# Kernel optimization log

Hardware: AMD Instinct MI355X
Metric: run time of the kernel (lower is better)

Reference implementation:

```python
import jax, jax.numpy as jnp
import numpy as np

T, B, V, E = 256, 128, 256, 512
NN = (1024, 1024)  # num_nodes per LSTM layer


def setup_inputs() -> dict:
    key = jax.random.key(0)
    ks = jax.random.split(key, 8)
    inputs = jax.random.normal(ks[0], (T, B, V), jnp.float32)
    emb = jax.random.normal(ks[1], (V, E), jnp.float32) * np.float32(np.sqrt(1.0 / V))
    w0 = jax.random.normal(ks[2], (E + NN[0], 4 * NN[0]), jnp.float32) * np.float32(np.sqrt(1.0 / (E + NN[0])))
    b0 = jnp.zeros((4 * NN[0],), jnp.float32)
    w1 = jax.random.normal(ks[3], (NN[0] + NN[1], 4 * NN[1]), jnp.float32) * np.float32(np.sqrt(1.0 / (NN[0] + NN[1])))
    b1 = jnp.zeros((4 * NN[1],), jnp.float32)
    out_w = jax.random.normal(ks[4], (NN[1], V), jnp.float32) * np.float32(np.sqrt(1.0 / NN[1]))
    out_b = jnp.zeros((V,), jnp.float32)
    return {"inputs": inputs, "embedding_matrix": emb,
            "lstm_w0": w0, "lstm_b0": b0, "lstm_w1": w1, "lstm_b1": b1,
            "out_w": out_w, "out_b": out_b}


def reference(inputs, embedding_matrix, lstm_w0, lstm_b0, lstm_w1, lstm_b1, out_w, out_b):
    Tn, Bn, _ = inputs.shape
    # _embed: (stacked one-hot) @ embedding_matrix -> [T, B, E]
    embs = jnp.einsum('tbv,ve->tbe', inputs, embedding_matrix)
    ws = (lstm_w0, lstm_w1)
    bs = (lstm_b0, lstm_b1)
    init_states = tuple((jnp.zeros((Bn, n), embs.dtype), jnp.zeros((Bn, n), embs.dtype)) for n in NN)

    def step(states, emb):
        out = emb
        new_states = []
        for i in range(len(NN)):
            h, c = states[i]
            n = NN[i]
            # concat([dropout(inp), h]) @ W + b ; dropout_keep_prob = 1.0 -> identity
            lin = jnp.concatenate([out, h], axis=1) @ ws[i] + bs[i]
            f = jax.nn.sigmoid(lin[:, :n])
            ig = jax.nn.sigmoid(lin[:, n:2 * n])
            o = jax.nn.sigmoid(lin[:, 2 * n:3 * n])
            g = jnp.tanh(lin[:, 3 * n:])
            c = f * c + ig * g
            h = o * jnp.tanh(c)
            out = h
            new_states.append((h, c))
        return tuple(new_states), out

    _, rnn_outputs = jax.lax.scan(step, init_states, embs)  # [T, B, NN[-1]]
    # output module: concat over time (axis 0) then single dense layer
    hs = rnn_outputs.reshape(Tn * Bn, NN[-1])
    logits = hs @ out_w + out_b  # [T*B, V]
    return logits
```

## Files before the change

### kernel.cpp

```cpp
#include <hip/hip_runtime.h>
#include <hip/hip_bf16.h>
#include <cstdint>
#include <cstddef>

#define T_STEPS 256
#define BATCH   128
#define VOCAB   256
#define EDIM    512
#define NH      1024
#define GDIM    4096
#define NST0    40
#define NST1    64

typedef __attribute__((ext_vector_type(8))) short short8;
typedef __attribute__((ext_vector_type(4))) float floatx4;

__device__ __forceinline__ float sigmoidf_(float x) { return 1.0f / (1.0f + __expf(-x)); }
__device__ __forceinline__ float tanhf_(float x)    { return 1.0f - 2.0f / (__expf(2.0f * x) + 1.0f); }

typedef __attribute__((address_space(1))) const unsigned int guint;
typedef __attribute__((address_space(3))) unsigned int luint;
__device__ __forceinline__ void load_lds16(const void* g, void* l) {
    __builtin_amdgcn_global_load_lds((guint*)g, (luint*)l, 16, 0, 0);
}

#define BM 128
#define BN 128
#define BK 16
__global__ __launch_bounds__(256) void sgemm_f32(
    const float* __restrict__ A, const float* __restrict__ B,
    float* __restrict__ C, int M, int N, int K)
{
    __shared__ float As[BK][BM + 4];
    __shared__ float Bs[BK][BN + 4];
    const int tid = threadIdx.x;
    const int tr = tid >> 4, tc = tid & 15;
    const int bm = blockIdx.y, bn = blockIdx.x;
    const float* Ab = A + (size_t)bm * BM * K;
    float acc[8][8];
    #pragma unroll
    for (int i = 0; i < 8; ++i)
        #pragma unroll
        for (int j = 0; j < 8; ++j) acc[i][j] = 0.f;
    for (int k0 = 0; k0 < K; k0 += BK) {
        #pragma unroll
        for (int l = 0; l < 2; ++l) {
            int idx = tid + l * 256;
            int row = idx >> 2, c4 = idx & 3;
            float4 v = *(const float4*)(Ab + (size_t)row * K + k0 + c4 * 4);
            As[c4 * 4 + 0][row] = v.x; As[c4 * 4 + 1][row] = v.y;
            As[c4 * 4 + 2][row] = v.z; As[c4 * 4 + 3][row] = v.w;
        }
        #pragma unroll
        for (int l = 0; l < 2; ++l) {
            int idx = tid + l * 256;
            int row = idx >> 5, c4 = idx & 31;
            *(float4*)&Bs[row][c4 * 4] = *(const float4*)(B + (size_t)(k0 + row) * N + bn * BN + c4 * 4);
        }
        __syncthreads();
        #pragma unroll
        for (int kk = 0; kk < BK; ++kk) {
            float4 a0 = *(const float4*)&As[kk][tr * 8];
            float4 a1 = *(const float4*)&As[kk][tr * 8 + 4];
            float4 b0 = *(const float4*)&Bs[kk][tc * 8];
            float4 b1 = *(const float4*)&Bs[kk][tc * 8 + 4];
            float av[8] = {a0.x, a0.y, a0.z, a0.w, a1.x, a1.y, a1.z, a1.w};
            float bv[8] = {b0.x, b0.y, b0.z, b0.w, b1.x, b1.y, b1.z, b1.w};
            #pragma unroll
            for (int i = 0; i < 8; ++i)
                #pragma unroll
                for (int j = 0; j < 8; ++j) acc[i][j] += av[i] * bv[j];
        }
        __syncthreads();
    }
    #pragma unroll
    for (int i = 0; i < 8; ++i) {
        size_t row = (size_t)bm * BM + tr * 8 + i;
        #pragma unroll
        for (int j = 0; j < 8; j += 4) {
            int col = bn * BN + tc * 8 + j;
            *(float4*)(C + row * N + col) =
                make_float4(acc[i][j], acc[i][j+1], acc[i][j+2], acc[i][j+3]);
        }
    }
}

__global__ __launch_bounds__(256) void transpose_to_bf16(
    const float* __restrict__ src, __hip_bfloat16* __restrict__ dst, int R, int C)
{
    __shared__ float t[32][33];
    int x = blockIdx.x * 32 + threadIdx.x;
    #pragma unroll
    for (int i = 0; i < 4; ++i) {
        int y = blockIdx.y * 32 + threadIdx.y + i * 8;
        t[threadIdx.y + i * 8][threadIdx.x] = src[(size_t)y * C + x];
    }
    __syncthreads();
    int x2 = blockIdx.y * 32 + threadIdx.x;
    #pragma unroll
    for (int i = 0; i < 4; ++i) {
        int y2 = blockIdx.x * 32 + threadIdx.y + i * 8;
        dst[(size_t)y2 * R + x2] = __float2bfloat16(t[threadIdx.x][threadIdx.y + i * 8]);
    }
}

__global__ __launch_bounds__(256) void pack_w2(
    const float* __restrict__ src, __hip_bfloat16* __restrict__ dst,
    int koff, int NSTEPS)
{
    __shared__ float t[64][33];
    const int tid = threadIdx.x;
    const int xt = blockIdx.x;
    const int kt = blockIdx.y;
    {
        int yl = tid >> 3;
        int x0 = (tid & 7) * 8;
        const float* p = src + (size_t)(kt * 32 + yl) * GDIM + xt * 64 + x0;
        float4 v0 = *(const float4*)p;
        float4 v1 = *(const float4*)(p + 4);
        t[x0 + 0][yl] = v0.x; t[x0 + 1][yl] = v0.y; t[x0 + 2][yl] = v0.z; t[x0 + 3][yl] = v0.w;
        t[x0 + 4][yl] = v1.x; t[x0 + 5][yl] = v1.y; t[x0 + 6][yl] = v1.z; t[x0 + 7][yl] = v1.w;
    }
    __syncthreads();
    {
        int ll = tid >> 2;
        int quad = tid & 3;
        int lincol = xt * 64 + ll;
        int g = lincol >> 10, n = lincol & 1023;
        int j = n >> 3, c = n & 7;
        int tt = g >> 1;
        int l16 = (g & 1) * 8 + c;
        int s = (koff >> 5) + kt;
        __hip_bfloat16 o[8];
        #pragma unroll
        for (int jj = 0; jj < 8; ++jj)
            o[jj] = __float2bfloat16(t[ll][quad * 8 + jj]);
        size_t off = ((((size_t)j * NSTEPS + s) * 2 + tt) * 64 + (size_t)quad * 16 + l16) * 8;
        *(uint4*)(dst + off) = *(const uint4*)o;
    }
}

__global__ __launch_bounds__(256) void convert_to_bf16(
    const float* __restrict__ src, __hip_bfloat16* __restrict__ dst, size_t n4)
{
    size_t i = (size_t)blockIdx.x * 256 + threadIdx.x;
    if (i < n4) {
        float4 v = *(const float4*)(src + i * 4);
        __hip_bfloat16 o[4] = {__float2bfloat16(v.x), __float2bfloat16(v.y),
                               __float2bfloat16(v.z), __float2bfloat16(v.w)};
        *(uint2*)(dst + i * 4) = *(uint2*)o;
    }
}

#define GKP 40
__global__ __launch_bounds__(256) void gemm_bt(
    const __hip_bfloat16* __restrict__ A, const __hip_bfloat16* __restrict__ Bt,
    const float* __restrict__ bias, float* __restrict__ C, int M, int N, int K)
{
    __shared__ __hip_bfloat16 As[128 * GKP];
    __shared__ __hip_bfloat16 Bs[128 * GKP];
    const int tid = threadIdx.x;
    const int wave = tid >> 6, lane = tid & 63;
    const int quad = lane >> 4, l16 = lane & 15;
    const int wm = (wave >> 1) * 64, wn = (wave & 1) * 64;
    const size_t Arow0 = (size_t)blockIdx.y * 128;
    const size_t Brow0 = (size_t)blockIdx.x * 128;
    floatx4 acc[4][4];
    #pragma unroll
    for (int i = 0; i < 4; ++i)
        #pragma unroll
        for (int j = 0; j < 4; ++j) acc[i][j] = (floatx4)0.f;

    for (int k0 = 0; k0 < K; k0 += 32) {
        #pragma unroll
        for (int l = 0; l < 2; ++l) {
            int idx = tid + l * 256;
            int row = idx >> 2, seg = idx & 3;
            *(uint4*)(As + row * GKP + seg * 8) =
                *(const uint4*)(A + (Arow0 + row) * K + k0 + seg * 8);
            *(uint4*)(Bs + row * GKP + seg * 8) =
                *(const uint4*)(Bt + (Brow0 + row) * K + k0 + seg * 8);
        }
        __syncthreads();
        short8 af[4], bf[4];
        #pragma unroll
        for (int i = 0; i < 4; ++i)
            af[i] = *(const short8*)(As + (wm + i * 16 + l16) * GKP + quad * 8);
        #pragma unroll
        for (int j = 0; j < 4; ++j)
            bf[j] = *(const short8*)(Bs + (wn + j * 16 + l16) * GKP + quad * 8);
        #pragma unroll
        for (int i = 0; i < 4; ++i)
            #pragma unroll
            for (int j = 0; j < 4; ++j)
                acc[i][j] = __builtin_amdgcn_mfma_f32_16x16x32_bf16(af[i], bf[j], acc[i][j], 0, 0, 0);
        __syncthreads();
    }
    #pragma unroll
    for (int i = 0; i < 4; ++i)
        #pragma unroll
        for (int j = 0; j < 4; ++j) {
            int col = (int)Brow0 + wn + j * 16 + l16;
            float bv = bias ? bias[col] : 0.f;
            #pragma unroll
            for (int r = 0; r < 4; ++r) {
                size_t row = Arow0 + wm + i * 16 + quad * 4 + r;
                C[row * N + col] = acc[i][j][r] + bv;
            }
        }
}

struct AfBuf { short8 a[3][8]; };

template<int NCF, int NCS>
__device__ __forceinline__ void chunks_pro(
    AfBuf& B, const __hip_bfloat16* __restrict__ pF,
    const __hip_bfloat16* __restrict__ pS)
{
    constexpr int NC = NCF + NCS;
    constexpr int D = (NC < 3) ? NC : 3;
    #pragma unroll
    for (int c = 0; c < D; ++c) {
        const __hip_bfloat16* pa = (c < NCF) ? (pF + (size_t)c * 256)
                                             : (pS + (size_t)(c - NCF) * 256);
        #pragma unroll
        for (int ss = 0; ss < 8; ++ss)
            B.a[c][ss] = *(const short8*)(pa + ss * 32);
    }
}

template<int NCF, int NCS, int WF, int WS>
__device__ __forceinline__ void chunks_main(
    AfBuf& B, const __hip_bfloat16* __restrict__ pF,
    const __hip_bfloat16* __restrict__ pS,
    const __hip_bfloat16* Wlds, int lane,
    floatx4& acc0, floatx4& acc1)
{
    constexpr int NC = NCF + NCS;
    #pragma unroll
    for (int c = 0; c < NC; ++c) {
        const int wc = (c < NCF) ? (WF + c) : (WS + (c - NCF));
        #pragma unroll
        for (int ss = 0; ss < 8; ++ss) {
            const int s = wc * 8 + ss;
            short8 bf0 = *(const short8*)&Wlds[s * 1024 + lane * 8];
            short8 bf1 = *(const short8*)&Wlds[s * 1024 + 512 + lane * 8];
            acc0 = __builtin_amdgcn_mfma_f32_16x16x32_bf16(B.a[c % 3][ss], bf0, acc0, 0, 0, 0);
            acc1 = __builtin_amdgcn_mfma_f32_16x16x32_bf16(B.a[c % 3][ss], bf1, acc1, 0, 0, 0);
        }
        if (c + 3 < NC) {
            const int cn = c + 3;
            const __hip_bfloat16* pa = (cn < NCF) ? (pF + (size_t)cn * 256)
                                                  : (pS + (size_t)(cn - NCF) * 256);
            #pragma unroll
            for (int ss = 0; ss < 8; ++ss)
                B.a[cn % 3][ss] = *(const short8*)(pa + ss * 32);
        }
    }
}

__global__ __launch_bounds__(512) void lstm_diag(
    const __hip_bfloat16* __restrict__ inbf,
    const __hip_bfloat16* __restrict__ Wpack0,
    const __hip_bfloat16* __restrict__ Wpack1,
    const float* __restrict__ b0, const float* __restrict__ b1,
    __hip_bfloat16* __restrict__ h0_cur,
    const __hip_bfloat16* __restrict__ h0_prev,
    float* __restrict__ c0, float* __restrict__ c1,
    __hip_bfloat16* __restrict__ H1all,
    int d)
{
    const int bid = blockIdx.x;
    const int layer = (bid >> 3) & 1;
    const int j = ((bid >> 4) << 3) | (bid & 7);
    if (layer == 0 && d >= T_STEPS) return;
    if (layer == 1 && d == 0) return;

    __shared__ __attribute__((aligned(16))) __hip_bfloat16 Wlds[65536];

    const int tid = threadIdx.x;
    const int wave = tid >> 6, lane = tid & 63;
    const int quad = lane >> 4, l16 = lane & 15;

    const __hip_bfloat16 *A0, *A1;
    int A0stride;
    const float* bb; float* cst; __hip_bfloat16* hout;
    bool first;
    if (layer == 0) {
        first = (d == 0);
        bb = b0; cst = c0;
        A0 = inbf + (size_t)d * (BATCH * VOCAB); A0stride = VOCAB;
        A1 = h0_prev;
        hout = h0_cur;
        const __hip_bfloat16* Wp = Wpack0 + (size_t)j * (NST0 * 1024);
        #pragma unroll
        for (int it = 0; it < 10; ++it)
            load_lds16(Wp + it * 4096 + tid * 8, Wlds + it * 4096 + tid * 8);
    } else {
        first = (d == 1);
        bb = b1; cst = c1;
        A0 = h0_prev; A0stride = NH;
        A1 = (d >= 2) ? (H1all + (size_t)(d - 2) * (BATCH * NH)) : h0_prev;
        hout = H1all + (size_t)(d - 1) * (BATCH * NH);
        const __hip_bfloat16* Wp = Wpack1 + (size_t)j * (NST1 * 1024);
        #pragma unroll
        for (int it = 0; it < 16; ++it)
            load_lds16(Wp + it * 4096 + tid * 8, Wlds + it * 4096 + tid * 8);
    }

    const int row = wave * 16 + l16;
    const __hip_bfloat16* pA0 = A0 + (size_t)row * A0stride + quad * 8;
    const __hip_bfloat16* pA1 = A1 + (size_t)row * NH + quad * 8;

    const int cc = j * 8 + (l16 & 7);
    float bv0 = bb[((l16 < 8) ? 0 : 1) * NH + cc];
    float bv1 = bb[((l16 < 8) ? 2 : 3) * NH + cc];
    float cold[4];
    {
        const int bbase = 16 * wave + quad * 4;
        #pragma unroll
        for (int r = 0; r < 4; ++r)
            cold[r] = first ? 0.f : cst[(size_t)(bbase + r) * NH + cc];
    }
    floatx4 acc0 = {bv0, bv0, bv0, bv0};
    floatx4 acc1 = {bv1, bv1, bv1, bv1};

    AfBuf B;
    __syncthreads();
    if (layer == 0) {
        if (first) { chunks_pro<1, 0>(B, pA0, pA0); chunks_main<1, 0, 0, 0>(B, pA0, pA0, Wlds, lane, acc0, acc1); }
        else       { chunks_pro<1, 4>(B, pA0, pA1); chunks_main<1, 4, 0, 1>(B, pA0, pA1, Wlds, lane, acc0, acc1); }
    } else {
        if (first) { chunks_pro<4, 0>(B, pA0, pA0); chunks_main<4, 0, 0, 0>(B, pA0, pA0, Wlds, lane, acc0, acc1); }
        else       { chunks_pro<4, 4>(B, pA1, pA0); chunks_main<4, 4, 4, 0>(B, pA1, pA0, Wlds, lane, acc0, acc1); }
    }

    #pragma unroll
    for (int r = 0; r < 4; ++r) {
        float a0 = acc0[r], a1 = acc1[r];
        float p0 = __shfl_xor(a0, 8, 64);
        float p1 = __shfl_xor(a1, 8, 64);
        if (l16 < 8) {
            int b = 16 * wave + quad * 4 + r;
            float f  = sigmoidf_(a0);
            float ig = sigmoidf_(p0);
            float oo = sigmoidf_(a1);
            float gg = tanhf_(p1);
            size_t idx = (size_t)b * NH + cc;
            float cn = f * cold[r] + ig * gg;
            float hn = oo * tanhf_(cn);
            cst[idx] = cn;
            hout[idx] = __float2bfloat16(hn);
        }
    }
}

__device__ __forceinline__ void spin_all_ge(const uint32_t* ep, uint32_t target,
                                            int lane, int wave) {
    asm volatile("" ::: "memory");
    if (wave == 0) {
        for (;;) {
            uint32_t a = __hip_atomic_load(&ep[lane], __ATOMIC_RELAXED, __HIP_MEMORY_SCOPE_AGENT);
            uint32_t b = __hip_atomic_load(&ep[lane + 64], __ATOMIC_RELAXED, __HIP_MEMORY_SCOPE_AGENT);
            if (__all(a >= target && b >= target)) break;
            __builtin_amdgcn_s_sleep(1);
        }
    }
    __builtin_amdgcn_s_barrier();
    asm volatile("" ::: "memory");
}

__device__ __forceinline__ void arrive_ep(uint32_t* slot, uint32_t val) {
    __syncthreads();
    asm volatile("" ::: "memory");
    if (threadIdx.x == 0)
        __hip_atomic_store(slot, val, __ATOMIC_RELAXED, __HIP_MEMORY_SCOPE_AGENT);
}

__global__ void zero_bar(uint32_t* p) { p[threadIdx.x] = 0; }

__global__ __launch_bounds__(512) void lstm_persist4(
    const __hip_bfloat16* __restrict__ inbf,
    const __hip_bfloat16* __restrict__ Wpack0,
    const __hip_bfloat16* __restrict__ Wpack1,
    const float* __restrict__ b0, const float* __restrict__ b1,
    __hip_bfloat16* __restrict__ H0all,
    __hip_bfloat16* __restrict__ H1all,
    uint32_t* __restrict__ bar)
{
    __shared__ __attribute__((aligned(16))) __hip_bfloat16 Wlds[65536];

    const int bid = blockIdx.x;
    const int layer = (bid >> 3) & 1;
    const int j = ((bid >> 4) << 3) | (bid & 7);
    const int tid = threadIdx.x;
    const int wave = tid >> 6, lane = tid & 63;
    const int quad = lane >> 4, l16 = lane & 15;

    uint32_t* ep0 = bar;
    uint32_t* ep1 = bar + 128;

    if (layer == 0) {
        const __hip_bfloat16* Wp = Wpack0 + (size_t)j * (NST0 * 1024);
        #pragma unroll
        for (int it = 0; it < 10; ++it)
            load_lds16(Wp + it * 4096 + tid * 8, Wlds + it * 4096 + tid * 8);
    } else {
        const __hip_bfloat16* Wp = Wpack1 + (size_t)j * (NST1 * 1024);
        #pragma unroll
        for (int it = 0; it < 16; ++it)
            load_lds16(Wp + it * 4096 + tid * 8, Wlds + it * 4096 + tid * 8);
    }
    __syncthreads();

    const int cc = j * 8 + (l16 & 7);
    const float* bb = layer ? b1 : b0;
    const float bv0 = bb[((l16 < 8) ? 0 : 1) * NH + cc];
    const float bv1 = bb[((l16 < 8) ? 2 : 3) * NH + cc];
    const int row = wave * 16 + l16;
    float creg[4] = {0.f, 0.f, 0.f, 0.f};

    if (layer == 0) {
        for (int d = 0; d < T_STEPS; ++d) {
            const bool first = (d == 0);
            const __hip_bfloat16* pA0 =
                inbf + (size_t)d * (BATCH * VOCAB) + (size_t)row * VOCAB + quad * 8;
            __hip_bfloat16* hout = H0all + (size_t)d * (BATCH * NH);
            floatx4 acc0 = {bv0, bv0, bv0, bv0};
            floatx4 acc1 = {bv1, bv1, bv1, bv1};
            AfBuf B;
            if (first) {
                chunks_pro<1, 0>(B, pA0, pA0);
                chunks_main<1, 0, 0, 0>(B, pA0, pA0, Wlds, lane, acc0, acc1);
            } else {
                spin_all_ge(ep0, (uint32_t)d, lane, wave);
                const __hip_bfloat16* pA1 =
                    H0all + (size_t)(d - 1) * (BATCH * NH) + (size_t)row * NH + quad * 8;
                chunks_pro<1, 4>(B, pA0, pA1);
                chunks_main<1, 4, 0, 1>(B, pA0, pA1, Wlds, lane, acc0, acc1);
            }
            #pragma unroll
            for (int r = 0; r < 4; ++r) {
                float a0 = acc0[r], a1 = acc1[r];
                float p0 = __shfl_xor(a0, 8, 64);
                float p1 = __shfl_xor(a1, 8, 64);
                float f  = sigmoidf_(a0);
                float ig = sigmoidf_(p0);
                float oo = sigmoidf_(a1);
                float gg = tanhf_(p1);
                float cn = f * (first ? 0.f : creg[r]) + ig * gg;
                if (l16 < 8) creg[r] = cn;
                float hn = oo * tanhf_(cn);
                union { __hip_bfloat16 h; unsigned short u; } cv;
                cv.h = __float2bfloat16(hn);
                unsigned int other = __shfl_xor((unsigned int)cv.u, 1, 64);
                if (l16 < 8 && !(l16 & 1)) {
                    unsigned int packed = (unsigned int)cv.u | (other << 16);
                    int b = 16 * wave + quad * 4 + r;
                    __hip_atomic_store((unsigned int*)&hout[(size_t)b * NH + cc],
                                       packed, __ATOMIC_RELAXED, __HIP_MEMORY_SCOPE_AGENT);
                }
            }
            arrive_ep(&ep0[j], (uint32_t)(d + 1));
        }
    } else {
        for (int d = 1; d <= T_STEPS; ++d) {
            const bool first = (d == 1);
            const __hip_bfloat16* pA0 =
                H0all + (size_t)(d - 1) * (BATCH * NH) + (size_t)row * NH + quad * 8;
            __hip_bfloat16* hout = H1all + (size_t)(d - 1) * (BATCH * NH);
            floatx4 acc0 = {bv0, bv0, bv0, bv0};
            floatx4 acc1 = {bv1, bv1, bv1, bv1};
            AfBuf B;
            if (first) {
                spin_all_ge(ep0, 1u, lane, wave);
                chunks_pro<4, 0>(B, pA0, pA0);
                chunks_main<4, 0, 0, 0>(B, pA0, pA0, Wlds, lane, acc0, acc1);
            } else {
                spin_all_ge(ep1, (uint32_t)(d - 1), lane, wave);
                const __hip_bfloat16* pA1 =
                    H1all + (size_t)(d - 2) * (BATCH * NH) + (size_t)row * NH + quad * 8;
                chunks_pro<4, 4>(B, pA1, pA0);
                spin_all_ge(ep0, (uint32_t)d, lane, wave);
                chunks_main<4, 4, 4, 0>(B, pA1, pA0, Wlds, lane, acc0, acc1);
            }
            #pragma unroll
            for (int r = 0; r < 4; ++r) {
                float a0 = acc0[r], a1 = acc1[r];
                float p0 = __shfl_xor(a0, 8, 64);
                float p1 = __shfl_xor(a1, 8, 64);
                float f  = sigmoidf_(a0);
                float ig = sigmoidf_(p0);
                float oo = sigmoidf_(a1);
                float gg = tanhf_(p1);
                float cn = f * (first ? 0.f : creg[r]) + ig * gg;
                if (l16 < 8) creg[r] = cn;
                float hn = oo * tanhf_(cn);
                union { __hip_bfloat16 h; unsigned short u; } cv;
                cv.h = __float2bfloat16(hn);
                unsigned int other = __shfl_xor((unsigned int)cv.u, 1, 64);
                if (l16 < 8 && !(l16 & 1)) {
                    unsigned int packed = (unsigned int)cv.u | (other << 16);
                    int b = 16 * wave + quad * 4 + r;
                    __hip_atomic_store((unsigned int*)&hout[(size_t)b * NH + cc],
                                       packed, __ATOMIC_RELAXED, __HIP_MEMORY_SCOPE_AGENT);
                }
            }
            arrive_ep(&ep1[j], (uint32_t)d);
        }
    }
}

extern "C" void kernel_launch(void* const* d_in, const int* in_sizes, int n_in,
                              void* d_out, int out_size, void* d_ws, size_t ws_size,
                              hipStream_t stream)
{
    const float* inputs = (const float*)d_in[0];
    const float* emb    = (const float*)d_in[1];
    const float* w0     = (const float*)d_in[2];
    const float* b0     = (const float*)d_in[3];
    const float* w1     = (const float*)d_in[4];
    const float* b1     = (const float*)d_in[5];
    const float* outw   = (const float*)d_in[6];
    const float* outb   = (const float*)d_in[7];
    float* out = (float*)d_out;

    char* ws = (char*)d_ws;
    size_t off = 0;
    auto take = [&](size_t bytes) { char* p = ws + off; off += (bytes + 255) & ~(size_t)255; return p; };
    float* Wcomb = (float*)take((size_t)VOCAB * GDIM * 4);
    __hip_bfloat16* Wpack0 = (__hip_bfloat16*)take((size_t)128 * NST0 * 1024 * 2);
    __hip_bfloat16* Wpack1 = (__hip_bfloat16*)take((size_t)128 * NST1 * 1024 * 2);
    __hip_bfloat16* outwt  = (__hip_bfloat16*)take((size_t)NH * VOCAB * 2);
    __hip_bfloat16* inbf   = (__hip_bfloat16*)take((size_t)T_STEPS * BATCH * VOCAB * 2);
    __hip_bfloat16* h0pp0  = (__hip_bfloat16*)take((size_t)BATCH * NH * 2);
    __hip_bfloat16* h0pp1  = (__hip_bfloat16*)take((size_t)BATCH * NH * 2);
    float* c0 = (float*)take((size_t)BATCH * NH * 4);
    float* c1 = (float*)take((size_t)BATCH * NH * 4);
    uint32_t* bar = (uint32_t*)take(1024);
    __hip_bfloat16* H1all  = (__hip_bfloat16*)take((size_t)T_STEPS * BATCH * NH * 2);
    __hip_bfloat16* H0all  = (__hip_bfloat16*)take((size_t)T_STEPS * BATCH * NH * 2);
    const bool ws_ok = (off <= ws_size);

    sgemm_f32<<<dim3(GDIM / BN, VOCAB / BM), 256, 0, stream>>>(
        emb, w0, Wcomb, VOCAB, GDIM, EDIM);
    pack_w2<<<dim3(64, VOCAB / 32), 256, 0, stream>>>(Wcomb, Wpack0, 0, NST0);
    pack_w2<<<dim3(64, NH / 32), 256, 0, stream>>>(w0 + (size_t)EDIM * GDIM, Wpack0, VOCAB, NST0);
    pack_w2<<<dim3(64, NH / 32), 256, 0, stream>>>(w1, Wpack1, 0, NST1);
    pack_w2<<<dim3(64, NH / 32), 256, 0, stream>>>(w1 + (size_t)NH * GDIM, Wpack1, NH, NST1);
    transpose_to_bf16<<<dim3(VOCAB / 32, NH / 32), dim3(32, 8), 0, stream>>>(
        outw, outwt, NH, VOCAB);
    {
        size_t n4 = (size_t)T_STEPS * BATCH * VOCAB / 4;
        convert_to_bf16<<<(int)((n4 + 255) / 256), 256, 0, stream>>>(inputs, inbf, n4);
    }
    zero_bar<<<1, 256, 0, stream>>>(bar);

    bool done = false;
    if (ws_ok) {
        void* args[] = { (void*)&inbf, (void*)&Wpack0, (void*)&Wpack1,
                         (void*)&b0, (void*)&b1,
                         (void*)&H0all, (void*)&H1all, (void*)&bar };
        hipError_t ce = hipLaunchCooperativeKernel(lstm_persist4, dim3(256), dim3(512),
                                                   args, 0u, stream);
        done = (ce == hipSuccess);
    }
    if (!done) {
        for (int d = 0; d <= T_STEPS; ++d) {
            __hip_bfloat16* hcur = (d & 1) ? h0pp1 : h0pp0;
            __hip_bfloat16* hprev = (d & 1) ? h0pp0 : h0pp1;
            lstm_diag<<<256, 512, 0, stream>>>(
                inbf, Wpack0, Wpack1, b0, b1, hcur, hprev, c0, c1, H1all, d);
        }
    }

    gemm_bt<<<dim3(VOCAB / 128, (T_STEPS * BATCH) / 128), 256, 0, stream>>>(
        H1all, outwt, outb, out, T_STEPS * BATCH, VOCAB, NH);
}
```

Before: 5.029 ms.

## Run both LSTM layers in every block with one wavefront-diagonal barrier

The persistent LSTM kernel stops splitting its 256 blocks into separate layer-0 and layer-1 groups of 8 hidden columns each. Every block now owns 4 hidden columns of both layers, keeps both weight slices in LDS (new pack_w4 layout with all four gates in one 16-wide MFMA tile), and steps a wavefront diagonal in which layer 0 handles step e and layer 1 handles step e-1. A single all-256-block epoch barrier per diagonal replaces the two producer/consumer flag arrays. The aim is to halve the MFMA count per block per layer and balance work across blocks. In exchange, each block does both layers serially, every barrier waits on all 256 blocks, and more weight-packing kernels run up front.

```diff
diff --git a/kernel.cpp b/kernel.cpp
--- a/kernel.cpp
+++ b/kernel.cpp
@@ -140,6 +140,41 @@
     }
 }
 
+__global__ __launch_bounds__(256) void pack_w4(
+    const float* __restrict__ src, __hip_bfloat16* __restrict__ dst,
+    int koff, int NSTEPS)
+{
+    __shared__ float t[64][33];
+    const int tid = threadIdx.x;
+    const int xt = blockIdx.x;
+    const int kt = blockIdx.y;
+    {
+        int yl = tid >> 3;
+        int x0 = (tid & 7) * 8;
+        const float* p = src + (size_t)(kt * 32 + yl) * GDIM + xt * 64 + x0;
+        float4 v0 = *(const float4*)p;
+        float4 v1 = *(const float4*)(p + 4);
+        t[x0 + 0][yl] = v0.x; t[x0 + 1][yl] = v0.y; t[x0 + 2][yl] = v0.z; t[x0 + 3][yl] = v0.w;
+        t[x0 + 4][yl] = v1.x; t[x0 + 5][yl] = v1.y; t[x0 + 6][yl] = v1.z; t[x0 + 7][yl] = v1.w;
+    }
+    __syncthreads();
+    {
+        int ll = tid >> 2;
+        int quad = tid & 3;
+        int lincol = xt * 64 + ll;
+        int g = lincol >> 10, n = lincol & 1023;
+        int j = n >> 2;
+        int l16 = g * 4 + (n & 3);
+        int s = (koff >> 5) + kt;
+        __hip_bfloat16 o[8];
+        #pragma unroll
+        for (int jj = 0; jj < 8; ++jj)
+            o[jj] = __float2bfloat16(t[ll][quad * 8 + jj]);
+        size_t off = (((size_t)j * NSTEPS + s) * 64 + (size_t)quad * 16 + l16) * 8;
+        *(uint4*)(dst + off) = *(const uint4*)o;
+    }
+}
+
 __global__ __launch_bounds__(256) void convert_to_bf16(
     const float* __restrict__ src, __hip_bfloat16* __restrict__ dst, size_t n4)
 {
@@ -247,6 +282,34 @@
             short8 bf1 = *(const short8*)&Wlds[s * 1024 + 512 + lane * 8];
             acc0 = __builtin_amdgcn_mfma_f32_16x16x32_bf16(B.a[c % 3][ss], bf0, acc0, 0, 0, 0);
             acc1 = __builtin_amdgcn_mfma_f32_16x16x32_bf16(B.a[c % 3][ss], bf1, acc1, 0, 0, 0);
+        }
+        if (c + 3 < NC) {
+            const int cn = c + 3;
+            const __hip_bfloat16* pa = (cn < NCF) ? (pF + (size_t)cn * 256)
+                                                  : (pS + (size_t)(cn - NCF) * 256);
+            #pragma unroll
+            for (int ss = 0; ss < 8; ++ss)
+                B.a[cn % 3][ss] = *(const short8*)(pa + ss * 32);
+        }
+    }
+}
+
+template<int NCF, int NCS, int WF, int WS>
+__device__ __forceinline__ void chunks1_main(
+    AfBuf& B, const __hip_bfloat16* __restrict__ pF,
+    const __hip_bfloat16* __restrict__ pS,
+    const __hip_bfloat16* Wlds, int lane,
+    floatx4& acc)
+{
+    constexpr int NC = NCF + NCS;
+    #pragma unroll
+    for (int c = 0; c < NC; ++c) {
+        const int wc = (c < NCF) ? (WF + c) : (WS + (c - NCF));
+        #pragma unroll
+        for (int ss = 0; ss < 8; ++ss) {
+            const int s = wc * 8 + ss;
+            short8 bf = *(const short8*)&Wlds[s * 512 + lane * 8];
+            acc = __builtin_amdgcn_mfma_f32_16x16x32_bf16(B.a[c % 3][ss], bf, acc, 0, 0, 0);
         }
         if (c + 3 < NC) {
             const int cn = c + 3;
@@ -355,15 +418,17 @@
     }
 }
 
-__device__ __forceinline__ void spin_all_ge(const uint32_t* ep, uint32_t target,
-                                            int lane, int wave) {
+__device__ __forceinline__ void spin_all_ge256(const uint32_t* ep, uint32_t target,
+                                               int lane, int wave) {
     asm volatile("" ::: "memory");
     if (wave == 0) {
         for (;;) {
-            uint32_t a = __hip_atomic_load(&ep[lane], __ATOMIC_RELAXED, __HIP_MEMORY_SCOPE_AGENT);
-            uint32_t b = __hip_atomic_load(&ep[lane + 64], __ATOMIC_RELAXED, __HIP_MEMORY_SCOPE_AGENT);
-            if (__all(a >= target && b >= target)) break;
-            __builtin_amdgcn_s_sleep(1);
+            uint32_t a = __hip_atomic_load(&ep[lane],       __ATOMIC_RELAXED, __HIP_MEMORY_SCOPE_AGENT);
+            uint32_t b = __hip_atomic_load(&ep[lane + 64],  __ATOMIC_RELAXED, __HIP_MEMORY_SCOPE_AGENT);
+            uint32_t c = __hip_atomic_load(&ep[lane + 128], __ATOMIC_RELAXED, __HIP_MEMORY_SCOPE_AGENT);
+            uint32_t d = __hip_atomic_load(&ep[lane + 192], __ATOMIC_RELAXED, __HIP_MEMORY_SCOPE_AGENT);
+            if (__all(a >= target && b >= target && c >= target && d >= target)) break;
+            __builtin_amdgcn_s_sleep(2);
         }
     }
     __builtin_amdgcn_s_barrier();
@@ -379,135 +444,129 @@
 
 __global__ void zero_bar(uint32_t* p) { p[threadIdx.x] = 0; }
 
-__global__ __launch_bounds__(512) void lstm_persist4(
+__global__ __launch_bounds__(512) void lstm_persist5(
     const __hip_bfloat16* __restrict__ inbf,
-    const __hip_bfloat16* __restrict__ Wpack0,
-    const __hip_bfloat16* __restrict__ Wpack1,
+    const __hip_bfloat16* __restrict__ Wp0,
+    const __hip_bfloat16* __restrict__ Wp1,
     const float* __restrict__ b0, const float* __restrict__ b1,
     __hip_bfloat16* __restrict__ H0all,
     __hip_bfloat16* __restrict__ H1all,
-    uint32_t* __restrict__ bar)
-{
-    __shared__ __attribute__((aligned(16))) __hip_bfloat16 Wlds[65536];
-
-    const int bid = blockIdx.x;
-    const int layer = (bid >> 3) & 1;
-    const int j = ((bid >> 4) << 3) | (bid & 7);
+    uint32_t* __restrict__ ep)
+{
+    __shared__ __attribute__((aligned(16))) __hip_bfloat16 W0lds[NST0 * 512];
+    __shared__ __attribute__((aligned(16))) __hip_bfloat16 W1lds[NST1 * 512];
+
+    const int j = blockIdx.x;
     const int tid = threadIdx.x;
     const int wave = tid >> 6, lane = tid & 63;
     const int quad = lane >> 4, l16 = lane & 15;
 
-    uint32_t* ep0 = bar;
-    uint32_t* ep1 = bar + 128;
-
-    if (layer == 0) {
-        const __hip_bfloat16* Wp = Wpack0 + (size_t)j * (NST0 * 1024);
-        #pragma unroll
-        for (int it = 0; it < 10; ++it)
-            load_lds16(Wp + it * 4096 + tid * 8, Wlds + it * 4096 + tid * 8);
-    } else {
-        const __hip_bfloat16* Wp = Wpack1 + (size_t)j * (NST1 * 1024);
-        #pragma unroll
-        for (int it = 0; it < 16; ++it)
-            load_lds16(Wp + it * 4096 + tid * 8, Wlds + it * 4096 + tid * 8);
+    {
+        const __hip_bfloat16* W0p = Wp0 + (size_t)j * (NST0 * 512);
+        #pragma unroll
+        for (int it = 0; it < 5; ++it)
+            load_lds16(W0p + it * 4096 + tid * 8, W0lds + it * 4096 + tid * 8);
+        const __hip_bfloat16* W1p = Wp1 + (size_t)j * (NST1 * 512);
+        #pragma unroll
+        for (int it = 0; it < 8; ++it)
+            load_lds16(W1p + it * 4096 + tid * 8, W1lds + it * 4096 + tid * 8);
     }
     __syncthreads();
 
-    const int cc = j * 8 + (l16 & 7);
-    const float* bb = layer ? b1 : b0;
-    const float bv0 = bb[((l16 < 8) ? 0 : 1) * NH + cc];
-    const float bv1 = bb[((l16 < 8) ? 2 : 3) * NH + cc];
+    const int gate = l16 >> 2, c4 = l16 & 3;
+    const int cc = j * 4 + c4;
+    const float bv0 = b0[gate * NH + j * 4 + c4];
+    const float bv1 = b1[gate * NH + j * 4 + c4];
     const int row = wave * 16 + l16;
-    float creg[4] = {0.f, 0.f, 0.f, 0.f};
-
-    if (layer == 0) {
-        for (int d = 0; d < T_STEPS; ++d) {
-            const bool first = (d == 0);
-            const __hip_bfloat16* pA0 =
-                inbf + (size_t)d * (BATCH * VOCAB) + (size_t)row * VOCAB + quad * 8;
-            __hip_bfloat16* hout = H0all + (size_t)d * (BATCH * NH);
-            floatx4 acc0 = {bv0, bv0, bv0, bv0};
-            floatx4 acc1 = {bv1, bv1, bv1, bv1};
+    float creg0[4] = {0.f, 0.f, 0.f, 0.f};
+    float creg1[4] = {0.f, 0.f, 0.f, 0.f};
+
+    for (int e = 0; e <= T_STEPS; ++e) {
+        if (e) spin_all_ge256(ep, (uint32_t)e, lane, wave);
+
+        if (e < T_STEPS) {
+            const bool first = (e == 0);
+            const __hip_bfloat16* pX =
+                inbf + (size_t)e * (BATCH * VOCAB) + (size_t)row * VOCAB + quad * 8;
+            const __hip_bfloat16* pH0 = first ? pX :
+                (H0all + (size_t)(e - 1) * (BATCH * NH) + (size_t)row * NH + quad * 8);
+            __hip_bfloat16* hout = H0all + (size_t)e * (BATCH * NH);
+            floatx4 acc = {bv0, bv0, bv0, bv0};
             AfBuf B;
             if (first) {
-                chunks_pro<1, 0>(B, pA0, pA0);
-                chunks_main<1, 0, 0, 0>(B, pA0, pA0, Wlds, lane, acc0, acc1);
+                chunks_pro<1, 0>(B, pX, pX);
+                chunks1_main<1, 0, 0, 0>(B, pX, pX, W0lds, lane, acc);
             } else {
-                spin_all_ge(ep0, (uint32_t)d, lane, wave);
-                const __hip_bfloat16* pA1 =
-                    H0all + (size_t)(d - 1) * (BATCH * NH) + (size_t)row * NH + quad * 8;
-                chunks_pro<1, 4>(B, pA0, pA1);
-                chunks_main<1, 4, 0, 1>(B, pA0, pA1, Wlds, lane, acc0, acc1);
+                chunks_pro<1, 4>(B, pX, pH0);
+                chunks1_main<1, 4, 0, 1>(B, pX, pH0, W0lds, lane, acc);
             }
             #pragma unroll
             for (int r = 0; r < 4; ++r) {
-                float a0 = acc0[r], a1 = acc1[r];
-                float p0 = __shfl_xor(a0, 8, 64);
-                float p1 = __shfl_xor(a1, 8, 64);
-                float f  = sigmoidf_(a0);
-                float ig = sigmoidf_(p0);
-                float oo = sigmoidf_(a1);
-                float gg = tanhf_(p1);
-                float cn = f * (first ? 0.f : creg[r]) + ig * gg;
-                if (l16 < 8) creg[r] = cn;
+                float v0  = acc[r];
+                float v4  = __shfl_xor(v0, 4, 64);
+                float v8  = __shfl_xor(v0, 8, 64);
+                float v12 = __shfl_xor(v4, 8, 64);
+                float f  = sigmoidf_(v0);
+                float ig = sigmoidf_(v4);
+                float oo = sigmoidf_(v8);
+                float gg = tanhf_(v12);
+                float cn = f * (first ? 0.f : creg0[r]) + ig * gg;
+                if (l16 < 4) creg0[r] = cn;
                 float hn = oo * tanhf_(cn);
                 union { __hip_bfloat16 h; unsigned short u; } cv;
                 cv.h = __float2bfloat16(hn);
                 unsigned int other = __shfl_xor((unsigned int)cv.u, 1, 64);
-                if (l16 < 8 && !(l16 & 1)) {
+                if (l16 < 4 && !(l16 & 1)) {
                     unsigned int packed = (unsigned int)cv.u | (other << 16);
                     int b = 16 * wave + quad * 4 + r;
                     __hip_atomic_store((unsigned int*)&hout[(size_t)b * NH + cc],
                                        packed, __ATOMIC_RELAXED, __HIP_MEMORY_SCOPE_AGENT);
                 }
             }
-            arrive_ep(&ep0[j], (uint32_t)(d + 1));
-        }
-    } else {
-        for (int d = 1; d <= T_STEPS; ++d) {
-            const bool first = (d == 1);
-            const __hip_bfloat16* pA0 =
-                H0all + (size_t)(d - 1) * (BATCH * NH) + (size_t)row * NH + quad * 8;
-            __hip_bfloat16* hout = H1all + (size_t)(d - 1) * (BATCH * NH);
-            floatx4 acc0 = {bv0, bv0, bv0, bv0};
-            floatx4 acc1 = {bv1, bv1, bv1, bv1};
+        }
+
+        if (e >= 1) {
+            const bool first = (e == 1);
+            const __hip_bfloat16* pH0 =
+                H0all + (size_t)(e - 1) * (BATCH * NH) + (size_t)row * NH + quad * 8;
+            const __hip_bfloat16* pH1 = first ? pH0 :
+                (H1all + (size_t)(e - 2) * (BATCH * NH) + (size_t)row * NH + quad * 8);
+            __hip_bfloat16* hout = H1all + (size_t)(e - 1) * (BATCH * NH);
+            floatx4 acc = {bv1, bv1, bv1, bv1};
             AfBuf B;
             if (first) {
-                spin_all_ge(ep0, 1u, lane, wave);
-                chunks_pro<4, 0>(B, pA0, pA0);
-                chunks_main<4, 0, 0, 0>(B, pA0, pA0, Wlds, lane, acc0, acc1);
+                chunks_pro<4, 0>(B, pH0, pH0);
+                chunks1_main<4, 0, 0, 0>(B, pH0, pH0, W1lds, lane, acc);
             } else {
-                spin_all_ge(ep1, (uint32_t)(d - 1), lane, wave);
-                const __hip_bfloat16* pA1 =
-                    H1all + (size_t)(d - 2) * (BATCH * NH) + (size_t)row * NH + quad * 8;
-                chunks_pro<4, 4>(B, pA1, pA0);
-                spin_all_ge(ep0, (uint32_t)d, lane, wave);
-                chunks_main<4, 4, 4, 0>(B, pA1, pA0, Wlds, lane, acc0, acc1);
+                chunks_pro<4, 4>(B, pH0, pH1);
+                chunks1_main<4, 4, 0, 4>(B, pH0, pH1, W1lds, lane, acc);
             }
             #pragma unroll
             for (int r = 0; r < 4; ++r) {
-                float a0 = acc0[r], a1 = acc1[r];
-                float p0 = __shfl_xor(a0, 8, 64);
-                float p1 = __shfl_xor(a1, 8, 64);
-                float f  = sigmoidf_(a0);
-                float ig = sigmoidf_(p0);
-                float oo = sigmoidf_(a1);
-                float gg = tanhf_(p1);
-                float cn = f * (first ? 0.f : creg[r]) + ig * gg;
-                if (l16 < 8) creg[r] = cn;
+                float v0  = acc[r];
+                float v4  = __shfl_xor(v0, 4, 64);
+                float v8  = __shfl_xor(v0, 8, 64);
+                float v12 = __shfl_xor(v4, 8, 64);
+                float f  = sigmoidf_(v0);
+                float ig = sigmoidf_(v4);
+                float oo = sigmoidf_(v8);
+                float gg = tanhf_(v12);
+                float cn = f * (first ? 0.f : creg1[r]) + ig * gg;
+                if (l16 < 4) creg1[r] = cn;
                 float hn = oo * tanhf_(cn);
                 union { __hip_bfloat16 h; unsigned short u; } cv;
                 cv.h = __float2bfloat16(hn);
                 unsigned int other = __shfl_xor((unsigned int)cv.u, 1, 64);
-                if (l16 < 8 && !(l16 & 1)) {
+                if (l16 < 4 && !(l16 & 1)) {
                     unsigned int packed = (unsigned int)cv.u | (other << 16);
                     int b = 16 * wave + quad * 4 + r;
                     __hip_atomic_store((unsigned int*)&hout[(size_t)b * NH + cc],
                                        packed, __ATOMIC_RELAXED, __HIP_MEMORY_SCOPE_AGENT);
                 }
             }
-            arrive_ep(&ep1[j], (uint32_t)d);
-        }
+        }
+
+        arrive_ep(&ep[j], (uint32_t)(e + 1));
     }
 }
 
@@ -540,6 +599,8 @@
     uint32_t* bar = (uint32_t*)take(1024);
     __hip_bfloat16* H1all  = (__hip_bfloat16*)take((size_t)T_STEPS * BATCH * NH * 2);
     __hip_bfloat16* H0all  = (__hip_bfloat16*)take((size_t)T_STEPS * BATCH * NH * 2);
+    __hip_bfloat16* Wp0n   = (__hip_bfloat16*)take((size_t)256 * NST0 * 512 * 2);
+    __hip_bfloat16* Wp1n   = (__hip_bfloat16*)take((size_t)256 * NST1 * 512 * 2);
     const bool ws_ok = (off <= ws_size);
 
     sgemm_f32<<<dim3(GDIM / BN, VOCAB / BM), 256, 0, stream>>>(
@@ -548,6 +609,12 @@
     pack_w2<<<dim3(64, NH / 32), 256, 0, stream>>>(w0 + (size_t)EDIM * GDIM, Wpack0, VOCAB, NST0);
     pack_w2<<<dim3(64, NH / 32), 256, 0, stream>>>(w1, Wpack1, 0, NST1);
     pack_w2<<<dim3(64, NH / 32), 256, 0, stream>>>(w1 + (size_t)NH * GDIM, Wpack1, NH, NST1);
+    if (ws_ok) {
+        pack_w4<<<dim3(64, VOCAB / 32), 256, 0, stream>>>(Wcomb, Wp0n, 0, NST0);
+        pack_w4<<<dim3(64, NH / 32), 256, 0, stream>>>(w0 + (size_t)EDIM * GDIM, Wp0n, VOCAB, NST0);
+        pack_w4<<<dim3(64, NH / 32), 256, 0, stream>>>(w1, Wp1n, 0, NST1);
+        pack_w4<<<dim3(64, NH / 32), 256, 0, stream>>>(w1 + (size_t)NH * GDIM, Wp1n, NH, NST1);
+    }
     transpose_to_bf16<<<dim3(VOCAB / 32, NH / 32), dim3(32, 8), 0, stream>>>(
         outw, outwt, NH, VOCAB);
     {
@@ -558,10 +625,10 @@
 
     bool done = false;
     if (ws_ok) {
-        void* args[] = { (void*)&inbf, (void*)&Wpack0, (void*)&Wpack1,
+        void* args[] = { (void*)&inbf, (void*)&Wp0n, (void*)&Wp1n,
                          (void*)&b0, (void*)&b1,
                          (void*)&H0all, (void*)&H1all, (void*)&bar };
-        hipError_t ce = hipLaunchCooperativeKernel(lstm_persist4, dim3(256), dim3(512),
+        hipError_t ce = hipLaunchCooperativeKernel(lstm_persist5, dim3(256), dim3(512),
                                                    args, 0u, stream);
         done = (ce == hipSuccess);
     }
```

Result: slower. 7.665 ms (+52.4%).

## Split recurrent matmul into segments to compute independent parts before barrier waits

Applied to the files above, without the earlier changes.

The fused A-operand pipeline is replaced by per-segment runs. In layer 0, the input-projection segment is computed before spinning on the previous step's h0. In layer 1, the h1 recurrence segment runs before waiting for the current h0. This moves independent MFMA work ahead of the cross-block synchronization to hide wait latency. The h stores also go out as 8-byte packed atomics instead of 4-byte ones. The cost is that the load pipeline restarts per segment, so there is less prefetch overlap between segments.

```diff
diff --git a/kernel.cpp b/kernel.cpp
--- a/kernel.cpp
+++ b/kernel.cpp
@@ -210,51 +210,33 @@
         }
 }
 
-struct AfBuf { short8 a[3][8]; };
-
-template<int NCF, int NCS>
-__device__ __forceinline__ void chunks_pro(
-    AfBuf& B, const __hip_bfloat16* __restrict__ pF,
-    const __hip_bfloat16* __restrict__ pS)
-{
-    constexpr int NC = NCF + NCS;
-    constexpr int D = (NC < 3) ? NC : 3;
-    #pragma unroll
-    for (int c = 0; c < D; ++c) {
-        const __hip_bfloat16* pa = (c < NCF) ? (pF + (size_t)c * 256)
-                                             : (pS + (size_t)(c - NCF) * 256);
-        #pragma unroll
-        for (int ss = 0; ss < 8; ++ss)
-            B.a[c][ss] = *(const short8*)(pa + ss * 32);
-    }
-}
-
-template<int NCF, int NCS, int WF, int WS>
-__device__ __forceinline__ void chunks_main(
-    AfBuf& B, const __hip_bfloat16* __restrict__ pF,
-    const __hip_bfloat16* __restrict__ pS,
+template<int NC, int W>
+__device__ __forceinline__ void seg_run(
+    const __hip_bfloat16* __restrict__ pA,
     const __hip_bfloat16* Wlds, int lane,
     floatx4& acc0, floatx4& acc1)
 {
-    constexpr int NC = NCF + NCS;
+    constexpr int D = (NC < 3) ? NC : 3;
+    short8 af[3][8];
+    #pragma unroll
+    for (int c = 0; c < D; ++c)
+        #pragma unroll
+        for (int ss = 0; ss < 8; ++ss)
+            af[c][ss] = *(const short8*)(pA + (size_t)c * 256 + ss * 32);
     #pragma unroll
     for (int c = 0; c < NC; ++c) {
-        const int wc = (c < NCF) ? (WF + c) : (WS + (c - NCF));
         #pragma unroll
         for (int ss = 0; ss < 8; ++ss) {
-            const int s = wc * 8 + ss;
+            const int s = (W + c) * 8 + ss;
             short8 bf0 = *(const short8*)&Wlds[s * 1024 + lane * 8];
             short8 bf1 = *(const short8*)&Wlds[s * 1024 + 512 + lane * 8];
-            acc0 = __builtin_amdgcn_mfma_f32_16x16x32_bf16(B.a[c % 3][ss], bf0, acc0, 0, 0, 0);
-            acc1 = __builtin_amdgcn_mfma_f32_16x16x32_bf16(B.a[c % 3][ss], bf1, acc1, 0, 0, 0);
+            acc0 = __builtin_amdgcn_mfma_f32_16x16x32_bf16(af[c % 3][ss], bf0, acc0, 0, 0, 0);
+            acc1 = __builtin_amdgcn_mfma_f32_16x16x32_bf16(af[c % 3][ss], bf1, acc1, 0, 0, 0);
         }
         if (c + 3 < NC) {
-            const int cn = c + 3;
-            const __hip_bfloat16* pa = (cn < NCF) ? (pF + (size_t)cn * 256)
-                                                  : (pS + (size_t)(cn - NCF) * 256);
             #pragma unroll
             for (int ss = 0; ss < 8; ++ss)
-                B.a[cn % 3][ss] = *(const short8*)(pa + ss * 32);
+                af[(c + 3) % 3][ss] = *(const short8*)(pA + (size_t)(c + 3) * 256 + ss * 32);
         }
     }
 }
@@ -325,14 +307,17 @@
     floatx4 acc0 = {bv0, bv0, bv0, bv0};
     floatx4 acc1 = {bv1, bv1, bv1, bv1};
 
-    AfBuf B;
     __syncthreads();
     if (layer == 0) {
-        if (first) { chunks_pro<1, 0>(B, pA0, pA0); chunks_main<1, 0, 0, 0>(B, pA0, pA0, Wlds, lane, acc0, acc1); }
-        else       { chunks_pro<1, 4>(B, pA0, pA1); chunks_main<1, 4, 0, 1>(B, pA0, pA1, Wlds, lane, acc0, acc1); }
+        seg_run<1, 0>(pA0, Wlds, lane, acc0, acc1);
+        if (!first) seg_run<4, 1>(pA1, Wlds, lane, acc0, acc1);
     } else {
-        if (first) { chunks_pro<4, 0>(B, pA0, pA0); chunks_main<4, 0, 0, 0>(B, pA0, pA0, Wlds, lane, acc0, acc1); }
-        else       { chunks_pro<4, 4>(B, pA1, pA0); chunks_main<4, 4, 4, 0>(B, pA1, pA0, Wlds, lane, acc0, acc1); }
+        if (first) {
+            seg_run<4, 0>(pA0, Wlds, lane, acc0, acc1);
+        } else {
+            seg_run<4, 4>(pA1, Wlds, lane, acc0, acc1);
+            seg_run<4, 0>(pA0, Wlds, lane, acc0, acc1);
+        }
     }
 
     #pragma unroll
@@ -379,7 +364,39 @@
 
 __global__ void zero_bar(uint32_t* p) { p[threadIdx.x] = 0; }
 
-__global__ __launch_bounds__(512) void lstm_persist4(
+__device__ __forceinline__ void epilogue_store(
+    floatx4 acc0, floatx4 acc1, float* creg, bool first,
+    int wave, int quad, int l16, int cc8base,
+    __hip_bfloat16* __restrict__ hout)
+{
+    #pragma unroll
+    for (int r = 0; r < 4; ++r) {
+        float a0 = acc0[r], a1 = acc1[r];
+        float p0 = __shfl_xor(a0, 8, 64);
+        float p1 = __shfl_xor(a1, 8, 64);
+        float f  = sigmoidf_(a0);
+        float ig = sigmoidf_(p0);
+        float oo = sigmoidf_(a1);
+        float gg = tanhf_(p1);
+        float cn = f * (first ? 0.f : creg[r]) + ig * gg;
+        if (l16 < 8) creg[r] = cn;
+        float hn = oo * tanhf_(cn);
+        union { __hip_bfloat16 h; unsigned short u; } cv;
+        cv.h = __float2bfloat16(hn);
+        unsigned int v1 = (unsigned int)cv.u |
+                          (__shfl_xor((unsigned int)cv.u, 1, 64) << 16);
+        unsigned int v2 = __shfl_xor(v1, 2, 64);
+        unsigned long long p8 = (unsigned long long)v1 |
+                                ((unsigned long long)v2 << 32);
+        if (l16 == 0 || l16 == 4) {
+            int b = 16 * wave + quad * 4 + r;
+            __hip_atomic_store((unsigned long long*)&hout[(size_t)b * NH + cc8base + l16],
+                               p8, __ATOMIC_RELAXED, __HIP_MEMORY_SCOPE_AGENT);
+        }
+    }
+}
+
+__global__ __launch_bounds__(512) void lstm_persist6(
     const __hip_bfloat16* __restrict__ inbf,
     const __hip_bfloat16* __restrict__ Wpack0,
     const __hip_bfloat16* __restrict__ Wpack1,
@@ -423,89 +440,38 @@
     if (layer == 0) {
         for (int d = 0; d < T_STEPS; ++d) {
             const bool first = (d == 0);
-            const __hip_bfloat16* pA0 =
+            const __hip_bfloat16* pX =
                 inbf + (size_t)d * (BATCH * VOCAB) + (size_t)row * VOCAB + quad * 8;
             __hip_bfloat16* hout = H0all + (size_t)d * (BATCH * NH);
             floatx4 acc0 = {bv0, bv0, bv0, bv0};
             floatx4 acc1 = {bv1, bv1, bv1, bv1};
-            AfBuf B;
-            if (first) {
-                chunks_pro<1, 0>(B, pA0, pA0);
-                chunks_main<1, 0, 0, 0>(B, pA0, pA0, Wlds, lane, acc0, acc1);
-            } else {
+            seg_run<1, 0>(pX, Wlds, lane, acc0, acc1);
+            if (!first) {
                 spin_all_ge(ep0, (uint32_t)d, lane, wave);
-                const __hip_bfloat16* pA1 =
+                const __hip_bfloat16* pH0 =
                     H0all + (size_t)(d - 1) * (BATCH * NH) + (size_t)row * NH + quad * 8;
-                chunks_pro<1, 4>(B, pA0, pA1);
-                chunks_main<1, 4, 0, 1>(B, pA0, pA1, Wlds, lane, acc0, acc1);
+                seg_run<4, 1>(pH0, Wlds, lane, acc0, acc1);
             }
-            #pragma unroll
-            for (int r = 0; r < 4; ++r) {
-                float a0 = acc0[r], a1 = acc1[r];
-                float p0 = __shfl_xor(a0, 8, 64);
-                float p1 = __shfl_xor(a1, 8, 64);
-                float f  = sigmoidf_(a0);
-                float ig = sigmoidf_(p0);
-                float oo = sigmoidf_(a1);
-                float gg = tanhf_(p1);
-                float cn = f * (first ? 0.f : creg[r]) + ig * gg;
-                if (l16 < 8) creg[r] = cn;
-                float hn = oo * tanhf_(cn);
-                union { __hip_bfloat16 h; unsigned short u; } cv;
-                cv.h = __float2bfloat16(hn);
-                unsigned int other = __shfl_xor((unsigned int)cv.u, 1, 64);
-                if (l16 < 8 && !(l16 & 1)) {
-                    unsigned int packed = (unsigned int)cv.u | (other << 16);
-                    int b = 16 * wave + quad * 4 + r;
-                    __hip_atomic_store((unsigned int*)&hout[(size_t)b * NH + cc],
-                                       packed, __ATOMIC_RELAXED, __HIP_MEMORY_SCOPE_AGENT);
-                }
-            }
+            epilogue_store(acc0, acc1, creg, first, wave, quad, l16, j * 8, hout);
             arrive_ep(&ep0[j], (uint32_t)(d + 1));
         }
     } else {
         for (int d = 1; d <= T_STEPS; ++d) {
             const bool first = (d == 1);
-            const __hip_bfloat16* pA0 =
-                H0all + (size_t)(d - 1) * (BATCH * NH) + (size_t)row * NH + quad * 8;
             __hip_bfloat16* hout = H1all + (size_t)(d - 1) * (BATCH * NH);
             floatx4 acc0 = {bv0, bv0, bv0, bv0};
             floatx4 acc1 = {bv1, bv1, bv1, bv1};
-            AfBuf B;
-            if (first) {
-                spin_all_ge(ep0, 1u, lane, wave);
-                chunks_pro<4, 0>(B, pA0, pA0);
-                chunks_main<4, 0, 0, 0>(B, pA0, pA0, Wlds, lane, acc0, acc1);
-            } else {
+            if (!first) {
                 spin_all_ge(ep1, (uint32_t)(d - 1), lane, wave);
-                const __hip_bfloat16* pA1 =
+                const __hip_bfloat16* pH1 =
                     H1all + (size_t)(d - 2) * (BATCH * NH) + (size_t)row * NH + quad * 8;
-                chunks_pro<4, 4>(B, pA1, pA0);
-                spin_all_ge(ep0, (uint32_t)d, lane, wave);
-                chunks_main<4, 4, 4, 0>(B, pA1, pA0, Wlds, lane, acc0, acc1);
+                seg_run<4, 4>(pH1, Wlds, lane, acc0, acc1);
             }
-            #pragma unroll
-            for (int r = 0; r < 4; ++r) {
-                float a0 = acc0[r], a1 = acc1[r];
-                float p0 = __shfl_xor(a0, 8, 64);
-                float p1 = __shfl_xor(a1, 8, 64);
-                float f  = sigmoidf_(a0);
-                float ig = sigmoidf_(p0);
-                float oo = sigmoidf_(a1);
-                float gg = tanhf_(p1);
-                float cn = f * (first ? 0.f : creg[r]) + ig * gg;
-                if (l16 < 8) creg[r] = cn;
-                float hn = oo * tanhf_(cn);
-                union { __hip_bfloat16 h; unsigned short u; } cv;
-                cv.h = __float2bfloat16(hn);
-                unsigned int other = __shfl_xor((unsigned int)cv.u, 1, 64);
-                if (l16 < 8 && !(l16 & 1)) {
-                    unsigned int packed = (unsigned int)cv.u | (other << 16);
-                    int b = 16 * wave + quad * 4 + r;
-                    __hip_atomic_store((unsigned int*)&hout[(size_t)b * NH + cc],
-                                       packed, __ATOMIC_RELAXED, __HIP_MEMORY_SCOPE_AGENT);
-                }
-            }
+            spin_all_ge(ep0, (uint32_t)d, lane, wave);
+            const __hip_bfloat16* pH0 =
+                H0all + (size_t)(d - 1) * (BATCH * NH) + (size_t)row * NH + quad * 8;
+            seg_run<4, 0>(pH0, Wlds, lane, acc0, acc1);
+            epilogue_store(acc0, acc1, creg, first, wave, quad, l16, j * 8, hout);
             arrive_ep(&ep1[j], (uint32_t)d);
         }
     }
@@ -561,7 +527,7 @@
         void* args[] = { (void*)&inbf, (void*)&Wpack0, (void*)&Wpack1,
                          (void*)&b0, (void*)&b1,
                          (void*)&H0all, (void*)&H1all, (void*)&bar };
-        hipError_t ce = hipLaunchCooperativeKernel(lstm_persist4, dim3(256), dim3(512),
+        hipError_t ce = hipLaunchCooperativeKernel(lstm_persist6, dim3(256), dim3(512),
                                                    args, 0u, stream);
         done = (ce == hipSuccess);
     }
```

Result: faster. 4.793 ms, median of 2 (-4.7%).
